# Performance work log

Hardware: AMD Instinct MI355X
Metric: run time of the kernel (lower is better)

Reference implementation:

```python
import jax, jax.numpy as jnp
import numpy as np

DIM = 512
HEADS = 8
NUM_KEYS = 256
TOPK = 16
B, T = 2, 2048
EPS = 1e-5  # BatchNorm1d default eps


def setup_inputs() -> dict:
    key = jax.random.key(0)
    ks = jax.random.split(key, 4)
    d_head = DIM // HEADS
    return {
        "x": jax.random.normal(ks[0], (B, T, DIM), jnp.float32),
        # nn.Linear(dim, dim, bias=False): weight (out, in), y = x @ W^T
        "Wq": jax.random.normal(ks[1], (DIM, DIM), jnp.float32) / np.sqrt(DIM),
        "gamma": jnp.ones((DIM,), jnp.float32),   # BatchNorm affine weight
        "beta": jnp.zeros((DIM,), jnp.float32),   # BatchNorm affine bias
        "keys": jax.random.normal(ks[2], (HEADS, NUM_KEYS, 2, d_head // 2), jnp.float32),
        "values": jax.random.normal(ks[3], (NUM_KEYS ** 2, DIM), jnp.float32),
    }


def reference(x, Wq, gamma, beta, keys, values):
    b, t, e = x.shape
    h, nk, k = HEADS, NUM_KEYS, TOPK
    # dropout layers are identity (p=0.0)
    q = jnp.einsum('bte,fe->btf', x, Wq)
    # MergeDims(BatchNorm1d) in training mode: batch stats over (b*t), biased var
    flat = q.reshape(-1, e)
    mean = flat.mean(axis=0)
    var = jnp.var(flat, axis=0)
    qn = ((flat - mean) * jax.lax.rsqrt(var + EPS) * gamma + beta).reshape(b, t, e)
    # chunk(2, dim=-1) then stack -> (2, b, t, h, d_head//2)
    qs = jnp.stack(jnp.split(qn, 2, axis=-1)).reshape(2, b, t, h, -1)
    dots = jnp.einsum('pbthd,hnpd->bthpn', qs, keys)  # (b,t,h,2,num_keys)
    scores, indices = jax.lax.top_k(dots, k)          # (b,t,h,2,k), sorted desc
    # faithful to source: chunk(2, dim=2) splits the HEAD axis
    h2 = h // 2
    s_a, s_b = scores[:, :, :h2], scores[:, :, h2:]    # (b,t,h/2,2,k)
    i_a, i_b = indices[:, :, :h2], indices[:, :, h2:]
    all_scores = (s_a[..., :, None] + s_b[..., None, :]).reshape(b, t, h, k * k)
    all_indices = (i_a[..., :, None] * nk + i_b[..., None, :]).reshape(b, t, h, k * k)
    final_scores, final_idx = jax.lax.top_k(all_scores, k)         # (b,t,h,k)
    value_indices = jnp.take_along_axis(all_indices, final_idx, axis=-1)
    attn = jax.nn.softmax(final_scores, axis=-1)
    vi = value_indices.reshape(-1, k * h)   # (b*t, k*h)
    w = attn.reshape(-1, k * h)
    # EmbeddingBag(mode='sum') with per_sample_weights
    out = jnp.einsum('nk,nkd->nd', w, values[vi])
    return out.reshape(b, t, e)
```

## Files before the change

kernel.cpp:

```cpp
#include <hip/hip_runtime.h>

#define NTOK 4096
#define EPS 1e-5f

__global__ void k_zero(float* __restrict__ stats) {
    int t = blockIdx.x * blockDim.x + threadIdx.x;
    if (t < 1024) stats[t] = 0.0f;
}

__global__ __launch_bounds__(256) void k_gemm(const float* __restrict__ A,
                                              const float* __restrict__ B,
                                              float* __restrict__ C) {
    __shared__ float As[32][68];
    __shared__ float Bs[32][68];
    const int tid  = threadIdx.x;
    const int row0 = blockIdx.x * 64;
    const int col0 = blockIdx.y * 64;
    const int lr = tid >> 3;
    const int lc = (tid & 7) << 2;
    const int tx = tid & 15;
    const int ty = tid >> 4;
    float acc[4][4] = {};
    for (int kc = 0; kc < 512; kc += 32) {
        float4 a0 = *(const float4*)(A + (row0 + lr)      * 512 + kc + lc);
        float4 a1 = *(const float4*)(A + (row0 + lr + 32) * 512 + kc + lc);
        float4 b0 = *(const float4*)(B + (col0 + lr)      * 512 + kc + lc);
        float4 b1 = *(const float4*)(B + (col0 + lr + 32) * 512 + kc + lc);
        __syncthreads();
        As[lc + 0][lr] = a0.x; As[lc + 1][lr] = a0.y; As[lc + 2][lr] = a0.z; As[lc + 3][lr] = a0.w;
        As[lc + 0][lr + 32] = a1.x; As[lc + 1][lr + 32] = a1.y; As[lc + 2][lr + 32] = a1.z; As[lc + 3][lr + 32] = a1.w;
        Bs[lc + 0][lr] = b0.x; Bs[lc + 1][lr] = b0.y; Bs[lc + 2][lr] = b0.z; Bs[lc + 3][lr] = b0.w;
        Bs[lc + 0][lr + 32] = b1.x; Bs[lc + 1][lr + 32] = b1.y; Bs[lc + 2][lr + 32] = b1.z; Bs[lc + 3][lr + 32] = b1.w;
        __syncthreads();
        #pragma unroll
        for (int k = 0; k < 32; ++k) {
            const float4 av = *(const float4*)&As[k][ty << 2];
            const float4 bv = *(const float4*)&Bs[k][tx << 2];
            const float a[4] = {av.x, av.y, av.z, av.w};
            const float b[4] = {bv.x, bv.y, bv.z, bv.w};
            #pragma unroll
            for (int i = 0; i < 4; ++i)
                #pragma unroll
                for (int j = 0; j < 4; ++j)
                    acc[i][j] += a[i] * b[j];
        }
    }
    #pragma unroll
    for (int i = 0; i < 4; ++i) {
        float4 v = make_float4(acc[i][0], acc[i][1], acc[i][2], acc[i][3]);
        *(float4*)(C + (row0 + ty * 4 + i) * 512 + col0 + (tx << 2)) = v;
    }
}

__global__ __launch_bounds__(256) void k_stats(const float* __restrict__ q,
                                               float* __restrict__ stats) {
    const int t  = threadIdx.x;
    const int r0 = blockIdx.x * 64;
    float s0 = 0.f, q0 = 0.f, s1 = 0.f, q1 = 0.f;
    for (int r = 0; r < 64; ++r) {
        const float a = q[(r0 + r) * 512 + t];
        const float b = q[(r0 + r) * 512 + 256 + t];
        s0 += a; q0 += a * a;
        s1 += b; q1 += b * b;
    }
    atomicAdd(&stats[t], s0);
    atomicAdd(&stats[t + 256], s1);
    atomicAdd(&stats[512 + t], q0);
    atomicAdd(&stats[512 + t + 256], q1);
}

__global__ void k_finalize(const float* __restrict__ stats, float* __restrict__ mr) {
    const int f = threadIdx.x;
    const float mean = stats[f] * (1.0f / 4096.0f);
    const float var  = stats[512 + f] * (1.0f / 4096.0f) - mean * mean;
    mr[f]       = mean;
    mr[512 + f] = rsqrtf(var + EPS);
}

__device__ __forceinline__ unsigned int fmono(float x) {
    const unsigned int u = __float_as_uint(x);
    return (u & 0x80000000u) ? ~u : (u | 0x80000000u);
}

__global__ __launch_bounds__(256, 4) void k_pkm(
    const float* __restrict__ q,
    const float* __restrict__ mr,
    const float* __restrict__ gamma,
    const float* __restrict__ beta,
    const float* __restrict__ keys,
    const float* __restrict__ values,
    float* __restrict__ out)
{
    __shared__ float qn[512];
    __shared__ float sTopS[16][16];
    __shared__ int   sTopI[16][16];
    __shared__ float wW[128];
    __shared__ int   wI[128];

    const int tok  = blockIdx.x;
    const int tid  = threadIdx.x;
    const int lane = tid & 63;
    const int wave = tid >> 6;

    {
        const float v0 = q[tok * 512 + tid];
        const float v1 = q[tok * 512 + 256 + tid];
        qn[tid]       = (v0 - mr[tid]) * mr[512 + tid] * gamma[tid] + beta[tid];
        qn[tid + 256] = (v1 - mr[tid + 256]) * mr[512 + tid + 256] * gamma[tid + 256] + beta[tid + 256];
    }
    __syncthreads();

    unsigned int cand[4][4];
    #pragma unroll
    for (int s4 = 0; s4 < 4; ++s4) {
        const int s = wave * 4 + s4;
        const int h = s >> 1;
        const int p = s & 1;
        const float4* qp4 = (const float4*)&qn[p * 256 + h * 32];
        #pragma unroll
        for (int j = 0; j < 4; ++j) {
            const int n = lane + 64 * j;
            const float4* kp4 = (const float4*)(keys + ((h * 256 + n) * 2 + p) * 32);
            float dot = 0.0f;
            #pragma unroll
            for (int d4 = 0; d4 < 8; ++d4) {
                const float4 kv = kp4[d4];
                const float4 qf = qp4[d4];
                dot += qf.x * kv.x + qf.y * kv.y + qf.z * kv.z + qf.w * kv.w;
            }
            cand[s4][j] = (fmono(dot) & 0xFFFFFF00u) | (unsigned int)(255 - n);
        }
    }

    unsigned int mywin1 = 0;
    #pragma unroll
    for (int it = 0; it < 16; ++it) {
        #pragma unroll
        for (int s4 = 0; s4 < 4; ++s4) {
            unsigned int lm = cand[s4][0];
            #pragma unroll
            for (int j = 1; j < 4; ++j) lm = (cand[s4][j] > lm) ? cand[s4][j] : lm;
            #pragma unroll
            for (int off = 32; off > 0; off >>= 1) {
                const unsigned int o = __shfl_xor(lm, off);
                lm = (o > lm) ? o : lm;
            }
            if (lane == s4 * 16 + it) mywin1 = lm;
            #pragma unroll
            for (int j = 0; j < 4; ++j) if (cand[s4][j] == lm) cand[s4][j] = 0u;
        }
    }
    {
        const int s = wave * 4 + (lane >> 4);
        const int h = s >> 1;
        const int p = s & 1;
        const int n = 255 - (int)(mywin1 & 0xFFu);
        const float4* qp4 = (const float4*)&qn[p * 256 + h * 32];
        const float4* kp4 = (const float4*)(keys + ((h * 256 + n) * 2 + p) * 32);
        float dot = 0.0f;
        #pragma unroll
        for (int d4 = 0; d4 < 8; ++d4) {
            const float4 kv = kp4[d4];
            const float4 qf = qp4[d4];
            dot += qf.x * kv.x + qf.y * kv.y + qf.z * kv.z + qf.w * kv.w;
        }
        sTopS[s][lane & 15] = dot;
        sTopI[s][lane & 15] = n;
    }
    __syncthreads();

    unsigned int c2[2][4];
    #pragma unroll
    for (int r2 = 0; r2 < 2; ++r2) {
        const int hh = wave * 2 + r2;
        const int ha = hh >> 1;
        const int p  = hh & 1;
        const int sa = ha * 2 + p;
        const int sb = (ha + 4) * 2 + p;
        const float sAv = sTopS[sa][lane >> 2];
        #pragma unroll
        for (int j = 0; j < 4; ++j) {
            const int c = lane * 4 + j;
            const float sc = sAv + sTopS[sb][c & 15];
            c2[r2][j] = (fmono(sc) & 0xFFFFFF00u) | (unsigned int)(255 - c);
        }
    }
    unsigned int mywin2 = 0;
    #pragma unroll
    for (int it = 0; it < 16; ++it) {
        #pragma unroll
        for (int r2 = 0; r2 < 2; ++r2) {
            unsigned int lm = c2[r2][0];
            #pragma unroll
            for (int j = 1; j < 4; ++j) lm = (c2[r2][j] > lm) ? c2[r2][j] : lm;
            #pragma unroll
            for (int off = 32; off > 0; off >>= 1) {
                const unsigned int o = __shfl_xor(lm, off);
                lm = (o > lm) ? o : lm;
            }
            if (lane == r2 * 16 + it) mywin2 = lm;
            #pragma unroll
            for (int j = 0; j < 4; ++j) if (c2[r2][j] == lm) c2[r2][j] = 0u;
        }
    }
    if (lane < 32) {
        const int r2 = lane >> 4;
        const int hh = wave * 2 + r2;
        const int ha = hh >> 1;
        const int p  = hh & 1;
        const int sa = ha * 2 + p;
        const int sb = (ha + 4) * 2 + p;
        const int c  = 255 - (int)(mywin2 & 0xFFu);
        const float sc = sTopS[sa][c >> 4] + sTopS[sb][c & 15];
        const float mx = __shfl(sc, lane & 48);
        const float e  = __expf(sc - mx);
        float ssum = e;
        #pragma unroll
        for (int off = 1; off < 16; off <<= 1) ssum += __shfl_xor(ssum, off);
        wW[hh * 16 + (lane & 15)] = e / ssum;
        wI[hh * 16 + (lane & 15)] = sTopI[sa][c >> 4] * 256 + sTopI[sb][c & 15];
    }
    __syncthreads();

    float2 acc = make_float2(0.0f, 0.0f);
    const float2* vb = (const float2*)values;
    #pragma unroll 8
    for (int k = 0; k < 128; ++k) {
        const float w   = wW[k];
        const int   idx = wI[k];
        const float2 v  = vb[idx * 256 + tid];
        acc.x += w * v.x;
        acc.y += w * v.y;
    }
    *(float2*)(out + tok * 512 + tid * 2) = acc;
}

extern "C" void kernel_launch(void* const* d_in, const int* in_sizes, int n_in,
                              void* d_out, int out_size, void* d_ws, size_t ws_size,
                              hipStream_t stream) {
    const float* x      = (const float*)d_in[0];
    const float* Wq     = (const float*)d_in[1];
    const float* gamma  = (const float*)d_in[2];
    const float* beta   = (const float*)d_in[3];
    const float* keys   = (const float*)d_in[4];
    const float* values = (const float*)d_in[5];
    float* out = (float*)d_out;

    float* q     = (float*)d_ws;
    float* stats = q + NTOK * 512;
    float* mr    = stats + 1024;

    k_zero<<<1, 1024, 0, stream>>>(stats);
    dim3 g1(NTOK / 64, 512 / 64);
    k_gemm<<<g1, 256, 0, stream>>>(x, Wq, q);
    k_stats<<<NTOK / 64, 256, 0, stream>>>(q, stats);
    k_finalize<<<1, 512, 0, stream>>>(stats, mr);
    k_pkm<<<NTOK, 256, 0, stream>>>(q, mr, gamma, beta, keys, values, out);
}
```

Before: 554.7 us.

## Fuse BatchNorm stats into GEMM epilogue and use DPP wave max in top-k

The per-column sum and sum-of-squares reduction moves into the GEMM epilogue, using shared-memory partial sums and atomics. This removes the separate stats kernel and its re-read of q. The wave-wide max in both top-k selection loops now uses DPP row operations plus a readlane of lane 63 instead of six xor shuffles, which lowers cross-lane latency in the hot selection loop. The cost is more atomics from the GEMM blocks, and the DPP sequence must produce a correct full-wave max broadcast.

```diff
diff --git a/kernel.cpp b/kernel.cpp
--- a/kernel.cpp
+++ b/kernel.cpp
@@ -10,7 +10,8 @@
 
 __global__ __launch_bounds__(256) void k_gemm(const float* __restrict__ A,
                                               const float* __restrict__ B,
-                                              float* __restrict__ C) {
+                                              float* __restrict__ C,
+                                              float* __restrict__ stats) {
     __shared__ float As[32][68];
     __shared__ float Bs[32][68];
     const int tid  = threadIdx.x;
@@ -50,23 +51,28 @@
         float4 v = make_float4(acc[i][0], acc[i][1], acc[i][2], acc[i][3]);
         *(float4*)(C + (row0 + ty * 4 + i) * 512 + col0 + (tx << 2)) = v;
     }
-}
-
-__global__ __launch_bounds__(256) void k_stats(const float* __restrict__ q,
-                                               float* __restrict__ stats) {
-    const int t  = threadIdx.x;
-    const int r0 = blockIdx.x * 64;
-    float s0 = 0.f, q0 = 0.f, s1 = 0.f, q1 = 0.f;
-    for (int r = 0; r < 64; ++r) {
-        const float a = q[(r0 + r) * 512 + t];
-        const float b = q[(r0 + r) * 512 + 256 + t];
-        s0 += a; q0 += a * a;
-        s1 += b; q1 += b * b;
-    }
-    atomicAdd(&stats[t], s0);
-    atomicAdd(&stats[t + 256], s1);
-    atomicAdd(&stats[512 + t], q0);
-    atomicAdd(&stats[512 + t + 256], q1);
+    __syncthreads();
+    float* redS = &As[0][0];
+    float* redQ = &Bs[0][0];
+    #pragma unroll
+    for (int j = 0; j < 4; ++j) {
+        const float s = acc[0][j] + acc[1][j] + acc[2][j] + acc[3][j];
+        const float qq = acc[0][j] * acc[0][j] + acc[1][j] * acc[1][j]
+                       + acc[2][j] * acc[2][j] + acc[3][j] * acc[3][j];
+        redS[ty * 64 + tx * 4 + j] = s;
+        redQ[ty * 64 + tx * 4 + j] = qq;
+    }
+    __syncthreads();
+    if (tid < 64) {
+        float a = 0.0f, b = 0.0f;
+        #pragma unroll
+        for (int t = 0; t < 16; ++t) {
+            a += redS[t * 64 + tid];
+            b += redQ[t * 64 + tid];
+        }
+        atomicAdd(&stats[col0 + tid], a);
+        atomicAdd(&stats[512 + col0 + tid], b);
+    }
 }
 
 __global__ void k_finalize(const float* __restrict__ stats, float* __restrict__ mr) {
@@ -80,6 +86,17 @@
 __device__ __forceinline__ unsigned int fmono(float x) {
     const unsigned int u = __float_as_uint(x);
     return (u & 0x80000000u) ? ~u : (u | 0x80000000u);
+}
+
+__device__ __forceinline__ unsigned int wave_max_u32(unsigned int m) {
+    unsigned int t;
+    t = (unsigned int)__builtin_amdgcn_update_dpp(0, (int)m, 0x121, 0xF, 0xF, true); m = t > m ? t : m;
+    t = (unsigned int)__builtin_amdgcn_update_dpp(0, (int)m, 0x122, 0xF, 0xF, true); m = t > m ? t : m;
+    t = (unsigned int)__builtin_amdgcn_update_dpp(0, (int)m, 0x124, 0xF, 0xF, true); m = t > m ? t : m;
+    t = (unsigned int)__builtin_amdgcn_update_dpp(0, (int)m, 0x128, 0xF, 0xF, true); m = t > m ? t : m;
+    t = (unsigned int)__builtin_amdgcn_update_dpp(0, (int)m, 0x142, 0xF, 0xF, true); m = t > m ? t : m;
+    t = (unsigned int)__builtin_amdgcn_update_dpp(0, (int)m, 0x143, 0xF, 0xF, true); m = t > m ? t : m;
+    return (unsigned int)__builtin_amdgcn_readlane((int)m, 63);
 }
 
 __global__ __launch_bounds__(256, 4) void k_pkm(
@@ -140,14 +157,10 @@
             unsigned int lm = cand[s4][0];
             #pragma unroll
             for (int j = 1; j < 4; ++j) lm = (cand[s4][j] > lm) ? cand[s4][j] : lm;
-            #pragma unroll
-            for (int off = 32; off > 0; off >>= 1) {
-                const unsigned int o = __shfl_xor(lm, off);
-                lm = (o > lm) ? o : lm;
-            }
-            if (lane == s4 * 16 + it) mywin1 = lm;
-            #pragma unroll
-            for (int j = 0; j < 4; ++j) if (cand[s4][j] == lm) cand[s4][j] = 0u;
+            const unsigned int win = wave_max_u32(lm);
+            if (lane == s4 * 16 + it) mywin1 = win;
+            #pragma unroll
+            for (int j = 0; j < 4; ++j) if (cand[s4][j] == win) cand[s4][j] = 0u;
         }
     }
     {
@@ -193,14 +206,10 @@
             unsigned int lm = c2[r2][0];
             #pragma unroll
             for (int j = 1; j < 4; ++j) lm = (c2[r2][j] > lm) ? c2[r2][j] : lm;
-            #pragma unroll
-            for (int off = 32; off > 0; off >>= 1) {
-                const unsigned int o = __shfl_xor(lm, off);
-                lm = (o > lm) ? o : lm;
-            }
-            if (lane == r2 * 16 + it) mywin2 = lm;
-            #pragma unroll
-            for (int j = 0; j < 4; ++j) if (c2[r2][j] == lm) c2[r2][j] = 0u;
+            const unsigned int win = wave_max_u32(lm);
+            if (lane == r2 * 16 + it) mywin2 = win;
+            #pragma unroll
+            for (int j = 0; j < 4; ++j) if (c2[r2][j] == win) c2[r2][j] = 0u;
         }
     }
     if (lane < 32) {
@@ -252,8 +261,7 @@
 
     k_zero<<<1, 1024, 0, stream>>>(stats);
     dim3 g1(NTOK / 64, 512 / 64);
-    k_gemm<<<g1, 256, 0, stream>>>(x, Wq, q);
-    k_stats<<<NTOK / 64, 256, 0, stream>>>(q, stats);
+    k_gemm<<<g1, 256, 0, stream>>>(x, Wq, q, stats);
     k_finalize<<<1, 512, 0, stream>>>(stats, mr);
     k_pkm<<<NTOK, 256, 0, stream>>>(q, mr, gamma, beta, keys, values, out);
 }
```

Measured after the change: 538.6 us. 1.03x faster.
